# Optimization experiments

Hardware: AMD Instinct MI355X
Metric: run time of the kernel (lower is better)

The kernel has to match this reference:

```python
import jax, jax.numpy as jnp
import numpy as np

N_NODES = 100000
N_EDGES = 1600000
IN_F = 32
HID = 128


def setup_inputs() -> dict:
    key = jax.random.key(0)
    ks = jax.random.split(key, 8)
    x = jax.random.normal(ks[0], (N_NODES, IN_F), dtype=jnp.float32)
    edge_index = jax.random.randint(ks[1], (2, N_EDGES), 0, N_NODES, dtype=jnp.int64)
    # Glorot-ish scaled weights
    W1 = jax.random.normal(ks[2], (IN_F, HID), dtype=jnp.float32) / np.sqrt(IN_F)
    b1 = jnp.zeros((HID,), dtype=jnp.float32)
    W2 = jax.random.normal(ks[3], (HID, HID), dtype=jnp.float32) / np.sqrt(HID)
    b2 = jnp.zeros((HID,), dtype=jnp.float32)
    W3 = jax.random.normal(ks[4], (HID, IN_F), dtype=jnp.float32) / np.sqrt(HID)
    b3 = jnp.zeros((IN_F,), dtype=jnp.float32)
    return {"x": x, "edge_index": edge_index, "W1": W1, "b1": b1,
            "W2": W2, "b2": b2, "W3": W3, "b3": b3}


def _gcn_norm(edge_index, n_nodes):
    # Add self-loops (PyG GCNConv default) and compute symmetric normalization
    loops = jnp.arange(n_nodes, dtype=edge_index.dtype)
    src = jnp.concatenate([edge_index[0], loops])
    dst = jnp.concatenate([edge_index[1], loops])
    ones = jnp.ones(src.shape[0], dtype=jnp.float32)
    deg = jax.ops.segment_sum(ones, dst, num_segments=n_nodes)
    deg_inv_sqrt = jnp.where(deg > 0, jax.lax.rsqrt(deg), 0.0)
    norm = deg_inv_sqrt[src] * deg_inv_sqrt[dst]  # [E + N]
    return src, dst, norm


def _gcn_conv(x, src, dst, norm, W, b, n_nodes):
    h = x @ W                                # [N, out] transform first (smaller msgs when out<in)
    msg = h[src] * norm[:, None]             # gather + edge-wise scale  [E+N, out]
    out = jax.ops.segment_sum(msg, dst, num_segments=n_nodes)  # scatter-add
    return out + b


def reference(x, edge_index, W1, b1, W2, b2, W3, b3):
    n = x.shape[0]
    src, dst, norm = _gcn_norm(edge_index, n)
    h = jax.nn.relu(_gcn_conv(x, src, dst, norm, W1, b1, n))
    h = jax.nn.relu(_gcn_conv(h, src, dst, norm, W2, b2, n))
    h = jax.nn.relu(_gcn_conv(h, src, dst, norm, W3, b3, n))
    return h
```

## Files before the change

kernel.cpp:

```cpp
#include <hip/hip_runtime.h>
#include <hip/hip_fp16.h>

#define N_NODES 100000
#define N_EDGES 1600000
#define IN_F 32
#define HID 128
#define BSHIFT 9
#define BSIZE 512
#define NBUCK 196
#define EPB 8192
#define NBB 196

typedef _Float16 half8 __attribute__((ext_vector_type(8)));
typedef float floatx4 __attribute__((ext_vector_type(4)));

static __device__ __forceinline__ void pack2(_Float16* dst, float a, float b) {
    union { _Float16 h[2]; unsigned u; } p;
    p.h[0] = (_Float16)a; p.h[1] = (_Float16)b;
    *(unsigned*)dst = p.u;
}


__global__ void k_zero_bcnt(int* __restrict__ bcnt) {
    if (threadIdx.x < 256) bcnt[threadIdx.x] = 0;
}

__global__ __launch_bounds__(256) void k_bcount(const int* __restrict__ dst,
                                                int* __restrict__ bcnt) {
    __shared__ int hist[256];
    hist[threadIdx.x] = 0;
    __syncthreads();
    const int e0 = blockIdx.x * EPB;
#pragma unroll 4
    for (int k = 0; k < 32; ++k) {
        int e = e0 + k * 256 + threadIdx.x;
        if (e < N_EDGES) atomicAdd(&hist[dst[e] >> BSHIFT], 1);
    }
    __syncthreads();
    int c = hist[threadIdx.x];
    if (c > 0) atomicAdd(&bcnt[threadIdx.x], c);
}

__global__ __launch_bounds__(256) void k_bscan(const int* __restrict__ bcnt,
                                               int* __restrict__ bbase,
                                               int* __restrict__ bcur) {
    __shared__ int s[256];
    int v = (threadIdx.x < NBUCK) ? bcnt[threadIdx.x] : 0;
    s[threadIdx.x] = v;
    __syncthreads();
    for (int off = 1; off < 256; off <<= 1) {
        int t = (threadIdx.x >= off) ? s[threadIdx.x - off] : 0;
        __syncthreads();
        s[threadIdx.x] += t;
        __syncthreads();
    }
    if (threadIdx.x < NBUCK) {
        int ex = s[threadIdx.x] - v;
        bbase[threadIdx.x] = ex;
        bcur[threadIdx.x]  = ex;
    }
    if (threadIdx.x == 0) bbase[NBUCK] = N_EDGES;
}

__global__ __launch_bounds__(256) void k_bucket(const int* __restrict__ src,
                                                const int* __restrict__ dst,
                                                int* __restrict__ bcur,
                                                unsigned* __restrict__ rec) {
    __shared__ int hist[256];
    __shared__ int lbase[256];
    const int e0 = blockIdx.x * EPB;
    hist[threadIdx.x] = 0;
    __syncthreads();

    unsigned rk[32]; short bk[32];
#pragma unroll
    for (int k = 0; k < 32; ++k) {
        int e = e0 + k * 256 + threadIdx.x;
        if (e < N_EDGES) {
            int d = dst[e];
            int b = d >> BSHIFT;
            bk[k] = (short)b;
            rk[k] = ((unsigned)src[e] << BSHIFT) | (unsigned)(d & (BSIZE - 1));
            atomicAdd(&hist[b], 1);
        } else bk[k] = -1;
    }
    __syncthreads();
    int c = hist[threadIdx.x];
    lbase[threadIdx.x] = (c > 0) ? atomicAdd(&bcur[threadIdx.x], c) : 0;
    __syncthreads();
    hist[threadIdx.x] = 0;
    __syncthreads();
#pragma unroll
    for (int k = 0; k < 32; ++k) {
        if (bk[k] >= 0) {
            int off = atomicAdd(&hist[bk[k]], 1);
            rec[lbase[bk[k]] + off] = rk[k];
        }
    }
}

__global__ __launch_bounds__(256) void k_fill3(const unsigned* __restrict__ rec,
                                               const int* __restrict__ bbase,
                                               int* __restrict__ ideg,
                                               int* __restrict__ cursor,
                                               int* __restrict__ col) {
    __shared__ int lcnt[BSIZE];
    __shared__ int lcur[BSIZE];
    __shared__ int s[256];
    const int b = blockIdx.x;
    const int n0 = b << BSHIFT;
    const int rbeg = bbase[b];
    const int rend = bbase[b + 1];

    lcnt[threadIdx.x] = 0;
    lcnt[threadIdx.x + 256] = 0;
    __syncthreads();
    for (int i = rbeg + threadIdx.x; i < rend; i += 256)
        atomicAdd(&lcnt[rec[i] & (BSIZE - 1)], 1);
    __syncthreads();

    int a0 = lcnt[2 * threadIdx.x], a1 = lcnt[2 * threadIdx.x + 1];
    int pv = a0 + a1;
    s[threadIdx.x] = pv;
    __syncthreads();
    for (int off = 1; off < 256; off <<= 1) {
        int t = (threadIdx.x >= off) ? s[threadIdx.x - off] : 0;
        __syncthreads();
        s[threadIdx.x] += t;
        __syncthreads();
    }
    int ex = s[threadIdx.x] - pv;
    lcur[2 * threadIdx.x]     = rbeg + ex;
    lcur[2 * threadIdx.x + 1] = rbeg + ex + a0;
    __syncthreads();

    for (int t = threadIdx.x; t < BSIZE; t += 256) {
        int n = n0 + t;
        if (n < N_NODES) {
            ideg[n]   = lcnt[t];
            cursor[n] = lcur[t];
        }
    }
    __syncthreads();
    for (int i = rbeg + threadIdx.x; i < rend; i += 256) {
        unsigned r = rec[i];
        int slot = atomicAdd(&lcur[r & (BSIZE - 1)], 1);
        col[slot] = (int)(r >> BSHIFT);
    }
}


__global__ void k_prescale(const float2* __restrict__ x, const int* __restrict__ ideg,
                           __half2* __restrict__ T) {
    int tid = blockIdx.x * 256 + threadIdx.x;
    if (tid >= N_NODES * 16) return;
    int i = tid >> 4;
    float dis = rsqrtf(1.0f + (float)ideg[i]);
    float2 v = x[tid];
    T[tid] = __floats2half2_rn(v.x * dis, v.y * dis);
}


__global__ __launch_bounds__(256) void k_gather32_pre(
    const int* __restrict__ cursor, const int* __restrict__ ideg,
    const int* __restrict__ col, const _Float16* __restrict__ T,
    _Float16* __restrict__ OUT) {
    const int lane = threadIdx.x & 63;
    const int slot = lane >> 2;
    const int fl   = lane & 3;
    const int wid  = blockIdx.x * 4 + (threadIdx.x >> 6);
    const int wstride = gridDim.x * 4;

    for (int node = wid; node < N_NODES; node += wstride) {
        int begin = cursor[node];
        int d     = ideg[node];
        int end   = begin + d;
        float acc[8];
        if (slot == 0) {
            half8 v = *(const half8*)(T + (size_t)node * IN_F + fl * 8);
#pragma unroll
            for (int i = 0; i < 8; ++i) acc[i] = (float)v[i];
        } else {
#pragma unroll
            for (int i = 0; i < 8; ++i) acc[i] = 0.f;
        }
        for (int e = begin; e < end; e += 16) {
            int ee = e + slot;
            if (ee < end) {
                int s = col[ee];
                half8 v = *(const half8*)(T + (size_t)s * IN_F + fl * 8);
#pragma unroll
                for (int i = 0; i < 8; ++i) acc[i] += (float)v[i];
            }
        }
#pragma unroll
        for (int m = 4; m < 64; m <<= 1)
#pragma unroll
            for (int i = 0; i < 8; ++i) acc[i] += __shfl_xor(acc[i], m, 64);
        if (slot == 0) {
            float dis = rsqrtf(1.0f + (float)d);
            half8 o;
#pragma unroll
            for (int i = 0; i < 8; ++i) o[i] = (_Float16)(acc[i] * dis);
            *(half8*)(OUT + (size_t)node * IN_F + fl * 8) = o;
        }
    }
}

__global__ __launch_bounds__(256) void k_gather32_fin(
    const int* __restrict__ cursor, const int* __restrict__ ideg,
    const int* __restrict__ col, const _Float16* __restrict__ T,
    const float* __restrict__ b, float* __restrict__ OUT) {
    const int lane = threadIdx.x & 63;
    const int slot = lane >> 2;
    const int fl   = lane & 3;
    const int wid  = blockIdx.x * 4 + (threadIdx.x >> 6);
    const int wstride = gridDim.x * 4;

    float4 bb0 = *(const float4*)(b + fl * 8);
    float4 bb1 = *(const float4*)(b + fl * 8 + 4);
    float bias[8] = {bb0.x, bb0.y, bb0.z, bb0.w, bb1.x, bb1.y, bb1.z, bb1.w};

    for (int node = wid; node < N_NODES; node += wstride) {
        int begin = cursor[node];
        int d     = ideg[node];
        int end   = begin + d;
        float acc[8];
        if (slot == 0) {
            half8 v = *(const half8*)(T + (size_t)node * IN_F + fl * 8);
#pragma unroll
            for (int i = 0; i < 8; ++i) acc[i] = (float)v[i];
        } else {
#pragma unroll
            for (int i = 0; i < 8; ++i) acc[i] = 0.f;
        }
        for (int e = begin; e < end; e += 16) {
            int ee = e + slot;
            if (ee < end) {
                int s = col[ee];
                half8 v = *(const half8*)(T + (size_t)s * IN_F + fl * 8);
#pragma unroll
                for (int i = 0; i < 8; ++i) acc[i] += (float)v[i];
            }
        }
#pragma unroll
        for (int m = 4; m < 64; m <<= 1)
#pragma unroll
            for (int i = 0; i < 8; ++i) acc[i] += __shfl_xor(acc[i], m, 64);
        if (slot == 0) {
            float dis = rsqrtf(1.0f + (float)d);
            float o[8];
#pragma unroll
            for (int i = 0; i < 8; ++i) {
                float v = acc[i] * dis + bias[i];
                o[i] = v > 0.f ? v : 0.f;
            }
            float* op = OUT + (size_t)node * IN_F + fl * 8;
            *(float4*)op       = make_float4(o[0], o[1], o[2], o[3]);
            *(float4*)(op + 4) = make_float4(o[4], o[5], o[6], o[7]);
        }
    }
}

__global__ __launch_bounds__(256) void k_gather128(
    const int* __restrict__ cursor, const int* __restrict__ ideg,
    const int* __restrict__ col, const _Float16* __restrict__ T,
    const float* __restrict__ b, _Float16* __restrict__ OUT) {
    const int lane = threadIdx.x & 63;
    const int slot = lane >> 4;
    const int fl   = lane & 15;
    const int wid  = blockIdx.x * 4 + (threadIdx.x >> 6);
    const int wstride = gridDim.x * 4;

    float4 bb0 = *(const float4*)(b + fl * 8);
    float4 bb1 = *(const float4*)(b + fl * 8 + 4);
    float bias[8] = {bb0.x, bb0.y, bb0.z, bb0.w, bb1.x, bb1.y, bb1.z, bb1.w};

    for (int node = wid; node < N_NODES; node += wstride) {
        int begin = cursor[node];
        int d     = ideg[node];
        int end   = begin + d;
        float acc[8];
        if (slot == 0) {
            half8 v = *(const half8*)(T + (size_t)node * HID + fl * 8);
#pragma unroll
            for (int i = 0; i < 8; ++i) acc[i] = (float)v[i];
        } else {
#pragma unroll
            for (int i = 0; i < 8; ++i) acc[i] = 0.f;
        }
        for (int e = begin; e < end; e += 8) {
            int ee0 = e + slot;
            int ee1 = e + 4 + slot;
            if (ee1 < end) {
                int s0 = col[ee0];
                int s1 = col[ee1];
                half8 v0 = *(const half8*)(T + (size_t)s0 * HID + fl * 8);
                half8 v1 = *(const half8*)(T + (size_t)s1 * HID + fl * 8);
#pragma unroll
                for (int i = 0; i < 8; ++i) acc[i] += (float)v0[i] + (float)v1[i];
            } else if (ee0 < end) {
                int s0 = col[ee0];
                half8 v0 = *(const half8*)(T + (size_t)s0 * HID + fl * 8);
#pragma unroll
                for (int i = 0; i < 8; ++i) acc[i] += (float)v0[i];
            }
        }
#pragma unroll
        for (int m = 16; m < 64; m <<= 1)
#pragma unroll
            for (int i = 0; i < 8; ++i) acc[i] += __shfl_xor(acc[i], m, 64);
        if (slot == 0) {
            float dis = rsqrtf(1.0f + (float)d);
            half8 o;
#pragma unroll
            for (int i = 0; i < 8; ++i) {
                float v = acc[i] * dis + bias[i];
                o[i] = (_Float16)(v > 0.f ? v : 0.f);
            }
            *(half8*)(OUT + (size_t)node * HID + fl * 8) = o;
        }
    }
}


__global__ __launch_bounds__(256) void k_xform1_mfma(
    const _Float16* __restrict__ z, const float* __restrict__ W,
    const float* __restrict__ bias, _Float16* __restrict__ Hh) {
    __shared__ _Float16 Wt[128 * 40];
    for (int idx = threadIdx.x; idx < 2048; idx += 256) {
        int n = idx & 127, k = (idx >> 7) * 2;
        pack2(&Wt[n * 40 + k], W[k * HID + n], W[(k + 1) * HID + n]);
    }
    __syncthreads();

    const int lane = threadIdx.x & 63;
    const int wave = threadIdx.x >> 6;
    const int m16 = lane & 15, quad = lane >> 4;
    const int row0 = blockIdx.x * 64 + wave * 16;
    if (row0 >= N_NODES) return;

    int arow = row0 + m16; if (arow >= N_NODES) arow = N_NODES - 1;
    half8 a = *(const half8*)(z + (size_t)arow * IN_F + quad * 8);

    floatx4 acc[8];
#pragma unroll
    for (int t = 0; t < 8; ++t) acc[t] = (floatx4){0.f, 0.f, 0.f, 0.f};
#pragma unroll
    for (int t = 0; t < 8; ++t) {
        half8 b = *(const half8*)&Wt[(t * 16 + m16) * 40 + quad * 8];
        acc[t] = __builtin_amdgcn_mfma_f32_16x16x32_f16(a, b, acc[t], 0, 0, 0);
    }
#pragma unroll
    for (int t = 0; t < 8; ++t) {
        int c = t * 16 + m16;
        float bj = bias[c];
#pragma unroll
        for (int r = 0; r < 4; ++r) {
            int row = row0 + quad * 4 + r;
            if (row < N_NODES) {
                float v = acc[t][r] + bj;
                Hh[(size_t)row * HID + c] = (_Float16)(v > 0.f ? v : 0.f);
            }
        }
    }
}

__global__ __launch_bounds__(256) void k_xform2_mfma(
    const _Float16* __restrict__ H, const float* __restrict__ W,
    const int* __restrict__ ideg, _Float16* __restrict__ T) {
    __shared__ _Float16 Wt[128 * 136];
    for (int idx = threadIdx.x; idx < 8192; idx += 256) {
        int n = idx & 127, k = (idx >> 7) * 2;
        pack2(&Wt[n * 136 + k], W[k * HID + n], W[(k + 1) * HID + n]);
    }
    __syncthreads();

    const int lane = threadIdx.x & 63;
    const int wave = threadIdx.x >> 6;
    const int m16 = lane & 15, quad = lane >> 4;
    const int row0 = blockIdx.x * 64 + wave * 16;
    if (row0 >= N_NODES) return;

    int arow = row0 + m16; if (arow >= N_NODES) arow = N_NODES - 1;
    const _Float16* hp = H + (size_t)arow * HID + quad * 8;
    half8 a[4];
#pragma unroll
    for (int kk = 0; kk < 4; ++kk) a[kk] = *(const half8*)(hp + kk * 32);

    floatx4 acc[8];
#pragma unroll
    for (int t = 0; t < 8; ++t) acc[t] = (floatx4){0.f, 0.f, 0.f, 0.f};
#pragma unroll
    for (int t = 0; t < 8; ++t) {
        const _Float16* wp = &Wt[(t * 16 + m16) * 136 + quad * 8];
#pragma unroll
        for (int kk = 0; kk < 4; ++kk) {
            half8 b = *(const half8*)(wp + kk * 32);
            acc[t] = __builtin_amdgcn_mfma_f32_16x16x32_f16(a[kk], b, acc[t], 0, 0, 0);
        }
    }
    float dis[4];
#pragma unroll
    for (int r = 0; r < 4; ++r) {
        int row = row0 + quad * 4 + r;
        dis[r] = (row < N_NODES) ? rsqrtf(1.0f + (float)ideg[row]) : 0.f;
    }
#pragma unroll
    for (int t = 0; t < 8; ++t) {
        int c = t * 16 + m16;
#pragma unroll
        for (int r = 0; r < 4; ++r) {
            int row = row0 + quad * 4 + r;
            if (row < N_NODES)
                T[(size_t)row * HID + c] = (_Float16)(acc[t][r] * dis[r]);
        }
    }
}

__global__ __launch_bounds__(256) void k_xform3_mfma(
    const _Float16* __restrict__ H, const float* __restrict__ W,
    const int* __restrict__ ideg, _Float16* __restrict__ T) {
    __shared__ _Float16 Wt[32 * 136];
    for (int idx = threadIdx.x; idx < 2048; idx += 256) {
        int n = idx & 31, k = (idx >> 5) * 2;
        pack2(&Wt[n * 136 + k], W[k * IN_F + n], W[(k + 1) * IN_F + n]);
    }
    __syncthreads();

    const int lane = threadIdx.x & 63;
    const int wave = threadIdx.x >> 6;
    const int m16 = lane & 15, quad = lane >> 4;
    const int row0 = blockIdx.x * 64 + wave * 16;
    if (row0 >= N_NODES) return;

    int arow = row0 + m16; if (arow >= N_NODES) arow = N_NODES - 1;
    const _Float16* hp = H + (size_t)arow * HID + quad * 8;
    half8 a[4];
#pragma unroll
    for (int kk = 0; kk < 4; ++kk) a[kk] = *(const half8*)(hp + kk * 32);

    floatx4 acc[2];
#pragma unroll
    for (int t = 0; t < 2; ++t) acc[t] = (floatx4){0.f, 0.f, 0.f, 0.f};
#pragma unroll
    for (int t = 0; t < 2; ++t) {
        const _Float16* wp = &Wt[(t * 16 + m16) * 136 + quad * 8];
#pragma unroll
        for (int kk = 0; kk < 4; ++kk) {
            half8 b = *(const half8*)(wp + kk * 32);
            acc[t] = __builtin_amdgcn_mfma_f32_16x16x32_f16(a[kk], b, acc[t], 0, 0, 0);
        }
    }
    float dis[4];
#pragma unroll
    for (int r = 0; r < 4; ++r) {
        int row = row0 + quad * 4 + r;
        dis[r] = (row < N_NODES) ? rsqrtf(1.0f + (float)ideg[row]) : 0.f;
    }
#pragma unroll
    for (int t = 0; t < 2; ++t) {
        int c = t * 16 + m16;
#pragma unroll
        for (int r = 0; r < 4; ++r) {
            int row = row0 + quad * 4 + r;
            if (row < N_NODES)
                T[(size_t)row * IN_F + c] = (_Float16)(acc[t][r] * dis[r]);
        }
    }
}


extern "C" void kernel_launch(void* const* d_in, const int* in_sizes, int n_in,
                              void* d_out, int out_size, void* d_ws, size_t ws_size,
                              hipStream_t stream) {
    const float* x  = (const float*)d_in[0];
    const int*   ei = (const int*)d_in[1];
    const float* W1 = (const float*)d_in[2];
    const float* b1 = (const float*)d_in[3];
    const float* W2 = (const float*)d_in[4];
    const float* b2 = (const float*)d_in[5];
    const float* W3 = (const float*)d_in[6];
    const float* b3 = (const float*)d_in[7];
    float* out = (float*)d_out;

    const int* src = ei;
    const int* dst = ei + N_EDGES;

    int*      ideg   = (int*)d_ws;
    int*      cursor = ideg + 102400;
    int*      bcnt   = cursor + 102400;
    int*      bbase  = bcnt + 256;
    int*      bcur   = bbase + 256;
    int*      col    = bcur + 256;
    unsigned* rec    = (unsigned*)(col + N_EDGES);
    _Float16* t1h    = (_Float16*)(rec + N_EDGES);
    _Float16* z      = t1h + (size_t)N_NODES * IN_F;
    _Float16* H1h    = z + (size_t)N_NODES * IN_F;
    _Float16* T2h    = H1h + (size_t)N_NODES * HID;
    _Float16* H2h    = T2h + (size_t)N_NODES * HID;

    const int xgrid = (N_NODES + 63) / 64;

    k_zero_bcnt<<<1, 256, 0, stream>>>(bcnt);
    k_bcount<<<NBB, 256, 0, stream>>>(dst, bcnt);
    k_bscan<<<1, 256, 0, stream>>>(bcnt, bbase, bcur);
    k_bucket<<<NBB, 256, 0, stream>>>(src, dst, bcur, rec);
    k_fill3<<<NBUCK, 256, 0, stream>>>(rec, bbase, ideg, cursor, col);

    k_prescale<<<(N_NODES * 16 + 255) / 256, 256, 0, stream>>>(
        (const float2*)x, ideg, (__half2*)t1h);
    k_gather32_pre<<<2048, 256, 0, stream>>>(cursor, ideg, col, t1h, z);
    k_xform1_mfma<<<xgrid, 256, 0, stream>>>(z, W1, b1, H1h);

    k_xform2_mfma<<<xgrid, 256, 0, stream>>>(H1h, W2, ideg, T2h);
    k_gather128<<<2048, 256, 0, stream>>>(cursor, ideg, col, T2h, b2, H2h);

    k_xform3_mfma<<<xgrid, 256, 0, stream>>>(H2h, W3, ideg, T2h);
    k_gather32_fin<<<2048, 256, 0, stream>>>(cursor, ideg, col, T2h, b3, out);
}
```

Baseline: 332.9 us.

## Fuse prescale into CSR fill and fuse dense transforms into gather kernels

Folds the input prescale into the CSR fill kernel, fuses the first dense transform (W1, bias, relu) into the 32-wide gather, and fuses the third transform (W3) into the 128-wide gather using per-wave shared-memory rows and scalar FMAs. A memset replaces the zeroing kernel. This removes several launches and the round trips of the intermediate z and H2 arrays through global memory. In exchange, the fused transforms use scalar ALU dot products instead of MFMA, and every block of the 2048-block gather grids reloads the weights into LDS.

```diff
diff --git a/kernel.cpp b/kernel.cpp
--- a/kernel.cpp
+++ b/kernel.cpp
@@ -21,10 +21,6 @@
 }
 
 
-__global__ void k_zero_bcnt(int* __restrict__ bcnt) {
-    if (threadIdx.x < 256) bcnt[threadIdx.x] = 0;
-}
-
 __global__ __launch_bounds__(256) void k_bcount(const int* __restrict__ dst,
                                                 int* __restrict__ bcnt) {
     __shared__ int hist[256];
@@ -99,11 +95,13 @@
     }
 }
 
-__global__ __launch_bounds__(256) void k_fill3(const unsigned* __restrict__ rec,
-                                               const int* __restrict__ bbase,
-                                               int* __restrict__ ideg,
-                                               int* __restrict__ cursor,
-                                               int* __restrict__ col) {
+__global__ __launch_bounds__(256) void k_fill3p(const unsigned* __restrict__ rec,
+                                                const int* __restrict__ bbase,
+                                                const float2* __restrict__ x,
+                                                int* __restrict__ ideg,
+                                                int* __restrict__ cursor,
+                                                int* __restrict__ col,
+                                                __half2* __restrict__ t1h) {
     __shared__ int lcnt[BSIZE];
     __shared__ int lcur[BSIZE];
     __shared__ int s[256];
@@ -141,6 +139,13 @@
             cursor[n] = lcur[t];
         }
     }
+    const int cnt = (n0 + BSIZE <= N_NODES) ? BSIZE : (N_NODES - n0);
+    for (int t = threadIdx.x; t < cnt * 16; t += 256) {
+        int ln = t >> 4;
+        float dis = rsqrtf(1.0f + (float)lcnt[ln]);
+        float2 v = x[(size_t)n0 * 16 + t];
+        t1h[(size_t)n0 * 16 + t] = __floats2half2_rn(v.x * dis, v.y * dis);
+    }
     __syncthreads();
     for (int i = rbeg + threadIdx.x; i < rend; i += 256) {
         unsigned r = rec[i];
@@ -150,26 +155,25 @@
 }
 
 
-__global__ void k_prescale(const float2* __restrict__ x, const int* __restrict__ ideg,
-                           __half2* __restrict__ T) {
-    int tid = blockIdx.x * 256 + threadIdx.x;
-    if (tid >= N_NODES * 16) return;
-    int i = tid >> 4;
-    float dis = rsqrtf(1.0f + (float)ideg[i]);
-    float2 v = x[tid];
-    T[tid] = __floats2half2_rn(v.x * dis, v.y * dis);
-}
-
-
-__global__ __launch_bounds__(256) void k_gather32_pre(
+__global__ __launch_bounds__(256) void k_g32_xf1(
     const int* __restrict__ cursor, const int* __restrict__ ideg,
     const int* __restrict__ col, const _Float16* __restrict__ T,
-    _Float16* __restrict__ OUT) {
+    const float* __restrict__ W1, const float* __restrict__ b1,
+    _Float16* __restrict__ H) {
+    __shared__ __half2 W1p[2048];
+    for (int idx = threadIdx.x; idx < 2048; idx += 256) {
+        int k2 = idx >> 7, j = idx & 127;
+        W1p[idx] = __floats2half2_rn(W1[(2 * k2) * HID + j], W1[(2 * k2 + 1) * HID + j]);
+    }
+    __syncthreads();
+
     const int lane = threadIdx.x & 63;
     const int slot = lane >> 2;
     const int fl   = lane & 3;
     const int wid  = blockIdx.x * 4 + (threadIdx.x >> 6);
     const int wstride = gridDim.x * 4;
+    const float bj0 = b1[lane];
+    const float bj1 = b1[lane + 64];
 
     for (int node = wid; node < N_NODES; node += wstride) {
         int begin = cursor[node];
@@ -197,17 +201,121 @@
         for (int m = 4; m < 64; m <<= 1)
 #pragma unroll
             for (int i = 0; i < 8; ++i) acc[i] += __shfl_xor(acc[i], m, 64);
+
+        float dis = rsqrtf(1.0f + (float)d);
+        float zz[4][8];
+#pragma unroll
+        for (int i = 0; i < 8; ++i) zz[0][i] = acc[i] * dis;
+#pragma unroll
+        for (int i = 0; i < 8; ++i) zz[1][i] = __shfl_xor(zz[0][i], 1, 64);
+#pragma unroll
+        for (int i = 0; i < 8; ++i) zz[2][i] = __shfl_xor(zz[0][i], 2, 64);
+#pragma unroll
+        for (int i = 0; i < 8; ++i) zz[3][i] = __shfl_xor(zz[0][i], 3, 64);
+
+        float s0 = 0.f, s1 = 0.f;
+#pragma unroll
+        for (int m = 0; m < 4; ++m) {
+            int f = fl ^ m;
+#pragma unroll
+            for (int i2 = 0; i2 < 4; ++i2) {
+                float2 w0 = __half22float2(W1p[(f * 4 + i2) * 128 + lane]);
+                float2 w1 = __half22float2(W1p[(f * 4 + i2) * 128 + lane + 64]);
+                s0 += zz[m][2 * i2] * w0.x + zz[m][2 * i2 + 1] * w0.y;
+                s1 += zz[m][2 * i2] * w1.x + zz[m][2 * i2 + 1] * w1.y;
+            }
+        }
+        float v0 = s0 + bj0, v1 = s1 + bj1;
+        H[(size_t)node * HID + lane]      = (_Float16)(v0 > 0.f ? v0 : 0.f);
+        H[(size_t)node * HID + lane + 64] = (_Float16)(v1 > 0.f ? v1 : 0.f);
+    }
+}
+
+
+__global__ __launch_bounds__(256) void k_g128_xf3(
+    const int* __restrict__ cursor, const int* __restrict__ ideg,
+    const int* __restrict__ col, const _Float16* __restrict__ T,
+    const float* __restrict__ b2, const float* __restrict__ W3,
+    _Float16* __restrict__ T3) {
+    __shared__ __half2 W3p[2048];
+    __shared__ float hrow[4][HID];
+    for (int idx = threadIdx.x; idx < 2048; idx += 256) {
+        int k2 = idx >> 5, j = idx & 31;
+        W3p[idx] = __floats2half2_rn(W3[(2 * k2) * IN_F + j], W3[(2 * k2 + 1) * IN_F + j]);
+    }
+    __syncthreads();
+
+    const int lane = threadIdx.x & 63;
+    const int slot = lane >> 4;
+    const int fl   = lane & 15;
+    const int wave = threadIdx.x >> 6;
+    const int wid  = blockIdx.x * 4 + wave;
+    const int wstride = gridDim.x * 4;
+    const int jcol  = lane & 31;
+    const int khalf = (lane >> 5) * 32;
+
+    float4 bb0 = *(const float4*)(b2 + fl * 8);
+    float4 bb1 = *(const float4*)(b2 + fl * 8 + 4);
+    float bias[8] = {bb0.x, bb0.y, bb0.z, bb0.w, bb1.x, bb1.y, bb1.z, bb1.w};
+
+    for (int node = wid; node < N_NODES; node += wstride) {
+        int begin = cursor[node];
+        int d     = ideg[node];
+        int end   = begin + d;
+        float acc[8];
         if (slot == 0) {
-            float dis = rsqrtf(1.0f + (float)d);
-            half8 o;
-#pragma unroll
-            for (int i = 0; i < 8; ++i) o[i] = (_Float16)(acc[i] * dis);
-            *(half8*)(OUT + (size_t)node * IN_F + fl * 8) = o;
-        }
-    }
-}
-
-__global__ __launch_bounds__(256) void k_gather32_fin(
+            half8 v = *(const half8*)(T + (size_t)node * HID + fl * 8);
+#pragma unroll
+            for (int i = 0; i < 8; ++i) acc[i] = (float)v[i];
+        } else {
+#pragma unroll
+            for (int i = 0; i < 8; ++i) acc[i] = 0.f;
+        }
+        for (int e = begin; e < end; e += 8) {
+            int ee0 = e + slot;
+            int ee1 = e + 4 + slot;
+            if (ee1 < end) {
+                int s0 = col[ee0];
+                int s1 = col[ee1];
+                half8 v0 = *(const half8*)(T + (size_t)s0 * HID + fl * 8);
+                half8 v1 = *(const half8*)(T + (size_t)s1 * HID + fl * 8);
+#pragma unroll
+                for (int i = 0; i < 8; ++i) acc[i] += (float)v0[i] + (float)v1[i];
+            } else if (ee0 < end) {
+                int s0 = col[ee0];
+                half8 v0 = *(const half8*)(T + (size_t)s0 * HID + fl * 8);
+#pragma unroll
+                for (int i = 0; i < 8; ++i) acc[i] += (float)v0[i];
+            }
+        }
+#pragma unroll
+        for (int m = 16; m < 64; m <<= 1)
+#pragma unroll
+            for (int i = 0; i < 8; ++i) acc[i] += __shfl_xor(acc[i], m, 64);
+
+        float dis = rsqrtf(1.0f + (float)d);
+        if (slot == 0) {
+#pragma unroll
+            for (int i = 0; i < 8; ++i) {
+                float v = acc[i] * dis + bias[i];
+                hrow[wave][fl * 8 + i] = v > 0.f ? v : 0.f;
+            }
+        }
+        float s = 0.f;
+#pragma unroll 8
+        for (int k2 = 0; k2 < 32; ++k2) {
+            float2 h2 = *(const float2*)&hrow[wave][(khalf + k2) * 2];
+            float2 wf = __half22float2(W3p[(khalf + k2) * 32 + jcol]);
+            s += h2.x * wf.x + h2.y * wf.y;
+        }
+        s += __shfl_xor(s, 32, 64);
+        if (lane < 32)
+            T3[(size_t)node * IN_F + jcol] = (_Float16)(s * dis);
+    }
+}
+
+
+__global__ __launch_bounds__(256) void k_g32fin(
     const int* __restrict__ cursor, const int* __restrict__ ideg,
     const int* __restrict__ col, const _Float16* __restrict__ T,
     const float* __restrict__ b, float* __restrict__ OUT) {
@@ -262,109 +370,6 @@
     }
 }
 
-__global__ __launch_bounds__(256) void k_gather128(
-    const int* __restrict__ cursor, const int* __restrict__ ideg,
-    const int* __restrict__ col, const _Float16* __restrict__ T,
-    const float* __restrict__ b, _Float16* __restrict__ OUT) {
-    const int lane = threadIdx.x & 63;
-    const int slot = lane >> 4;
-    const int fl   = lane & 15;
-    const int wid  = blockIdx.x * 4 + (threadIdx.x >> 6);
-    const int wstride = gridDim.x * 4;
-
-    float4 bb0 = *(const float4*)(b + fl * 8);
-    float4 bb1 = *(const float4*)(b + fl * 8 + 4);
-    float bias[8] = {bb0.x, bb0.y, bb0.z, bb0.w, bb1.x, bb1.y, bb1.z, bb1.w};
-
-    for (int node = wid; node < N_NODES; node += wstride) {
-        int begin = cursor[node];
-        int d     = ideg[node];
-        int end   = begin + d;
-        float acc[8];
-        if (slot == 0) {
-            half8 v = *(const half8*)(T + (size_t)node * HID + fl * 8);
-#pragma unroll
-            for (int i = 0; i < 8; ++i) acc[i] = (float)v[i];
-        } else {
-#pragma unroll
-            for (int i = 0; i < 8; ++i) acc[i] = 0.f;
-        }
-        for (int e = begin; e < end; e += 8) {
-            int ee0 = e + slot;
-            int ee1 = e + 4 + slot;
-            if (ee1 < end) {
-                int s0 = col[ee0];
-                int s1 = col[ee1];
-                half8 v0 = *(const half8*)(T + (size_t)s0 * HID + fl * 8);
-                half8 v1 = *(const half8*)(T + (size_t)s1 * HID + fl * 8);
-#pragma unroll
-                for (int i = 0; i < 8; ++i) acc[i] += (float)v0[i] + (float)v1[i];
-            } else if (ee0 < end) {
-                int s0 = col[ee0];
-                half8 v0 = *(const half8*)(T + (size_t)s0 * HID + fl * 8);
-#pragma unroll
-                for (int i = 0; i < 8; ++i) acc[i] += (float)v0[i];
-            }
-        }
-#pragma unroll
-        for (int m = 16; m < 64; m <<= 1)
-#pragma unroll
-            for (int i = 0; i < 8; ++i) acc[i] += __shfl_xor(acc[i], m, 64);
-        if (slot == 0) {
-            float dis = rsqrtf(1.0f + (float)d);
-            half8 o;
-#pragma unroll
-            for (int i = 0; i < 8; ++i) {
-                float v = acc[i] * dis + bias[i];
-                o[i] = (_Float16)(v > 0.f ? v : 0.f);
-            }
-            *(half8*)(OUT + (size_t)node * HID + fl * 8) = o;
-        }
-    }
-}
-
-
-__global__ __launch_bounds__(256) void k_xform1_mfma(
-    const _Float16* __restrict__ z, const float* __restrict__ W,
-    const float* __restrict__ bias, _Float16* __restrict__ Hh) {
-    __shared__ _Float16 Wt[128 * 40];
-    for (int idx = threadIdx.x; idx < 2048; idx += 256) {
-        int n = idx & 127, k = (idx >> 7) * 2;
-        pack2(&Wt[n * 40 + k], W[k * HID + n], W[(k + 1) * HID + n]);
-    }
-    __syncthreads();
-
-    const int lane = threadIdx.x & 63;
-    const int wave = threadIdx.x >> 6;
-    const int m16 = lane & 15, quad = lane >> 4;
-    const int row0 = blockIdx.x * 64 + wave * 16;
-    if (row0 >= N_NODES) return;
-
-    int arow = row0 + m16; if (arow >= N_NODES) arow = N_NODES - 1;
-    half8 a = *(const half8*)(z + (size_t)arow * IN_F + quad * 8);
-
-    floatx4 acc[8];
-#pragma unroll
-    for (int t = 0; t < 8; ++t) acc[t] = (floatx4){0.f, 0.f, 0.f, 0.f};
-#pragma unroll
-    for (int t = 0; t < 8; ++t) {
-        half8 b = *(const half8*)&Wt[(t * 16 + m16) * 40 + quad * 8];
-        acc[t] = __builtin_amdgcn_mfma_f32_16x16x32_f16(a, b, acc[t], 0, 0, 0);
-    }
-#pragma unroll
-    for (int t = 0; t < 8; ++t) {
-        int c = t * 16 + m16;
-        float bj = bias[c];
-#pragma unroll
-        for (int r = 0; r < 4; ++r) {
-            int row = row0 + quad * 4 + r;
-            if (row < N_NODES) {
-                float v = acc[t][r] + bj;
-                Hh[(size_t)row * HID + c] = (_Float16)(v > 0.f ? v : 0.f);
-            }
-        }
-    }
-}
 
 __global__ __launch_bounds__(256) void k_xform2_mfma(
     const _Float16* __restrict__ H, const float* __restrict__ W,
@@ -414,58 +419,6 @@
             int row = row0 + quad * 4 + r;
             if (row < N_NODES)
                 T[(size_t)row * HID + c] = (_Float16)(acc[t][r] * dis[r]);
-        }
-    }
-}
-
-__global__ __launch_bounds__(256) void k_xform3_mfma(
-    const _Float16* __restrict__ H, const float* __restrict__ W,
-    const int* __restrict__ ideg, _Float16* __restrict__ T) {
-    __shared__ _Float16 Wt[32 * 136];
-    for (int idx = threadIdx.x; idx < 2048; idx += 256) {
-        int n = idx & 31, k = (idx >> 5) * 2;
-        pack2(&Wt[n * 136 + k], W[k * IN_F + n], W[(k + 1) * IN_F + n]);
-    }
-    __syncthreads();
-
-    const int lane = threadIdx.x & 63;
-    const int wave = threadIdx.x >> 6;
-    const int m16 = lane & 15, quad = lane >> 4;
-    const int row0 = blockIdx.x * 64 + wave * 16;
-    if (row0 >= N_NODES) return;
-
-    int arow = row0 + m16; if (arow >= N_NODES) arow = N_NODES - 1;
-    const _Float16* hp = H + (size_t)arow * HID + quad * 8;
-    half8 a[4];
-#pragma unroll
-    for (int kk = 0; kk < 4; ++kk) a[kk] = *(const half8*)(hp + kk * 32);
-
-    floatx4 acc[2];
-#pragma unroll
-    for (int t = 0; t < 2; ++t) acc[t] = (floatx4){0.f, 0.f, 0.f, 0.f};
-#pragma unroll
-    for (int t = 0; t < 2; ++t) {
-        const _Float16* wp = &Wt[(t * 16 + m16) * 136 + quad * 8];
-#pragma unroll
-        for (int kk = 0; kk < 4; ++kk) {
-            half8 b = *(const half8*)(wp + kk * 32);
-            acc[t] = __builtin_amdgcn_mfma_f32_16x16x32_f16(a[kk], b, acc[t], 0, 0, 0);
-        }
-    }
-    float dis[4];
-#pragma unroll
-    for (int r = 0; r < 4; ++r) {
-        int row = row0 + quad * 4 + r;
-        dis[r] = (row < N_NODES) ? rsqrtf(1.0f + (float)ideg[row]) : 0.f;
-    }
-#pragma unroll
-    for (int t = 0; t < 2; ++t) {
-        int c = t * 16 + m16;
-#pragma unroll
-        for (int r = 0; r < 4; ++r) {
-            int row = row0 + quad * 4 + r;
-            if (row < N_NODES)
-                T[(size_t)row * IN_F + c] = (_Float16)(acc[t][r] * dis[r]);
         }
     }
 }
@@ -495,27 +448,21 @@
     int*      col    = bcur + 256;
     unsigned* rec    = (unsigned*)(col + N_EDGES);
     _Float16* t1h    = (_Float16*)(rec + N_EDGES);
-    _Float16* z      = t1h + (size_t)N_NODES * IN_F;
-    _Float16* H1h    = z + (size_t)N_NODES * IN_F;
+    _Float16* H1h    = t1h + (size_t)N_NODES * IN_F;
     _Float16* T2h    = H1h + (size_t)N_NODES * HID;
-    _Float16* H2h    = T2h + (size_t)N_NODES * HID;
-
-    const int xgrid = (N_NODES + 63) / 64;
-
-    k_zero_bcnt<<<1, 256, 0, stream>>>(bcnt);
+    _Float16* T3h    = T2h + (size_t)N_NODES * HID;
+
+    hipMemsetAsync(bcnt, 0, 256 * sizeof(int), stream);
     k_bcount<<<NBB, 256, 0, stream>>>(dst, bcnt);
     k_bscan<<<1, 256, 0, stream>>>(bcnt, bbase, bcur);
     k_bucket<<<NBB, 256, 0, stream>>>(src, dst, bcur, rec);
-    k_fill3<<<NBUCK, 256, 0, stream>>>(rec, bbase, ideg, cursor, col);
-
-    k_prescale<<<(N_NODES * 16 + 255) / 256, 256, 0, stream>>>(
-        (const float2*)x, ideg, (__half2*)t1h);
-    k_gather32_pre<<<2048, 256, 0, stream>>>(cursor, ideg, col, t1h, z);
-    k_xform1_mfma<<<xgrid, 256, 0, stream>>>(z, W1, b1, H1h);
-
-    k_xform2_mfma<<<xgrid, 256, 0, stream>>>(H1h, W2, ideg, T2h);
-    k_gather128<<<2048, 256, 0, stream>>>(cursor, ideg, col, T2h, b2, H2h);
-
-    k_xform3_mfma<<<xgrid, 256, 0, stream>>>(H2h, W3, ideg, T2h);
-    k_gather32_fin<<<2048, 256, 0, stream>>>(cursor, ideg, col, T2h, b3, out);
-}
+    k_fill3p<<<NBUCK, 256, 0, stream>>>(rec, bbase, (const float2*)x,
+                                        ideg, cursor, col, (__half2*)t1h);
+
+    k_g32_xf1<<<2048, 256, 0, stream>>>(cursor, ideg, col, t1h, W1, b1, H1h);
+
+    k_xform2_mfma<<<(N_NODES + 63) / 64, 256, 0, stream>>>(H1h, W2, ideg, T2h);
+    k_g128_xf3<<<2048, 256, 0, stream>>>(cursor, ideg, col, T2h, b2, W3, T3h);
+
+    k_g32fin<<<2048, 256, 0, stream>>>(cursor, ideg, col, T3h, b3, out);
+}
```

After: 353.2 us. 6.1% more time.
